# Performance work log

Hardware: AMD Instinct MI355X
Metric: run time of the kernel (lower is better)

## Reference

```python
import jax, jax.numpy as jnp
import numpy as np

D_MODEL = 1024
NHEAD = 16
HEAD_DIM = D_MODEL // NHEAD
SCALE = HEAD_DIM ** (-0.5)


def setup_inputs() -> dict:
    key = jax.random.key(0)
    k1, k2, k3 = jax.random.split(key, 3)
    B, T, C = 2, 2048, D_MODEL
    x = jax.random.normal(k1, (B, T, C), dtype=jnp.float32)
    W_qkv = jax.random.normal(k2, (3 * C, C), dtype=jnp.float32) * (C ** -0.5)
    b_qkv = jnp.zeros((3 * C,), dtype=jnp.float32)
    W_out = jax.random.normal(k3, (C, C), dtype=jnp.float32) * (C ** -0.5)
    b_out = jnp.zeros((C,), dtype=jnp.float32)
    return {"x": x, "W_qkv": W_qkv, "b_qkv": b_qkv, "W_out": W_out, "b_out": b_out}


def reference(x, W_qkv, b_qkv, W_out, b_out):
    B, T, C = x.shape
    H, hd = NHEAD, HEAD_DIM
    qkv = x @ W_qkv.T + b_qkv
    qkv = qkv.reshape(B, T, 3, H, hd).transpose(2, 0, 3, 1, 4)
    q, k, v = qkv[0], qkv[1], qkv[2]
    # scaled dot-product scores: (B,H,T,T)
    attn = jnp.einsum('bhqd,bhkd->bhqk', q, k) * SCALE
    # causal mask (is_causal=True): lower-triangular allowed
    causal = jnp.tril(jnp.ones((T, T), dtype=bool))
    attn = jnp.where(causal[None, None, :, :], attn, -jnp.inf)
    attn = jax.nn.softmax(attn, axis=-1)
    # (B,H,T,hd) -> (B,T,C)
    out = jnp.einsum('bhqk,bhkd->bhqd', attn, v)
    out = out.transpose(0, 2, 1, 3).reshape(B, T, C)
    out = out @ W_out.T + b_out
    return out
```

## Files before the change

kernel.cpp:

```cpp
#include <hip/hip_runtime.h>
#include <hip/hip_bf16.h>
#include <stdint.h>

#define D_MODEL 1024
#define NHEAD   16
#define HEAD_DIM 64
#define BATCH   2
#define SEQ     2048
#define M_TOK   (BATCH*SEQ)
#define N_QKV   (3*D_MODEL)
#define KDIM    1024
#define Q_SCALE (0.125f * 1.44269504088896f)

typedef __bf16 bf16_t;
typedef bf16_t bf16x8 __attribute__((ext_vector_type(8)));
typedef bf16_t bf16x4 __attribute__((ext_vector_type(4)));
typedef float  f32x4  __attribute__((ext_vector_type(4)));
typedef float  f32x16 __attribute__((ext_vector_type(16)));
typedef unsigned u32x4 __attribute__((ext_vector_type(4)));

__device__ __forceinline__ void gl_lds16(const void* g, void* l) {
    __builtin_amdgcn_global_load_lds(
        (__attribute__((address_space(1))) void*)(void*)(const_cast<void*>(g)),
        (__attribute__((address_space(3))) void*)l, 16, 0, 0);
}

__device__ __forceinline__ unsigned cvtpk_bf16(float a, float b) {
    unsigned r;
    asm("v_cvt_pk_bf16_f32 %0, %1, %2" : "=v"(r) : "v"(a), "v"(b));
    return r;
}

#define N4_X  (M_TOK * KDIM / 4)
#define N4_W1 (N_QKV * KDIM / 4)
#define N4_W2 (D_MODEL * KDIM / 4)
__global__ void convert_all(const float* __restrict__ x,
                            const float* __restrict__ w1,
                            const float* __restrict__ w2,
                            bf16_t* __restrict__ ox,
                            bf16_t* __restrict__ o1,
                            bf16_t* __restrict__ o2) {
    int t = blockIdx.x * blockDim.x + threadIdx.x;
    const float* src;
    bf16_t* dst;
    int off;
    if (t < N4_X)                { src = x;  dst = ox; off = t; }
    else if (t < N4_X + N4_W1)   { src = w1; dst = o1; off = t - N4_X; }
    else                         { src = w2; dst = o2; off = t - N4_X - N4_W1; }
    float4 v = reinterpret_cast<const float4*>(src)[off];
    bf16x4 o = { (bf16_t)v.x, (bf16_t)v.y, (bf16_t)v.z, (bf16_t)v.w };
    reinterpret_cast<bf16x4*>(dst)[off] = o;
}

template <int MODE, int TN>
__global__ __launch_bounds__(256) void gemm_bt(
    const bf16_t* __restrict__ A,
    const bf16_t* __restrict__ Bw,
    const float*  __restrict__ bias,
    int N,
    bf16_t* __restrict__ qkv_out,
    bf16_t* __restrict__ vt_out,
    float*  __restrict__ f32_out)
{
    constexpr int NJ = TN / 32;
    __shared__ bf16_t As[128 * 64];
    __shared__ bf16_t Bs[TN * 64];

    const int cpx = gridDim.x >> 3;
    const int bid = (blockIdx.x & 7) * cpx + (blockIdx.x >> 3);

    const int nbn = N / TN;
    const int bm = bid / nbn;
    const int bn = bid % nbn;
    const int m0 = bm * 128, n0 = bn * TN;
    const int tid = threadIdx.x, wave = tid >> 6, lane = tid & 63;
    const int wr = wave >> 1, wc = wave & 1;

    f32x4 acc[4][NJ] = {};

    const int srow = lane >> 3;
    const int scol = ((lane & 7) ^ srow) * 8;
    const bf16_t* gA0 = A  + (size_t)(m0 + wave * 32 + srow) * KDIM + scol;
    const bf16_t* gB0 = Bw + (size_t)(n0 + wave * (TN / 4) + srow) * KDIM + scol;
    bf16_t* lA0 = &As[(wave * 32) * 64];
    bf16_t* lB0 = &Bs[(wave * (TN / 4)) * 64];

    const int fr = lane & 15;
    const int kq = lane >> 4;

    for (int k0 = 0; k0 < KDIM; k0 += 64) {
#pragma unroll
        for (int c = 0; c < 4; c++)
            gl_lds16(gA0 + (size_t)(c * 8) * KDIM + k0, lA0 + (c * 8) * 64);
#pragma unroll
        for (int c = 0; c < TN / 32; c++)
            gl_lds16(gB0 + (size_t)(c * 8) * KDIM + k0, lB0 + (c * 8) * 64);
        __syncthreads();

        bf16x8 af[2][4], bfr[2][NJ];
#pragma unroll
        for (int kk = 0; kk < 2; kk++) {
            const int ch = (((kk << 2) | kq) ^ (fr & 7)) * 8;
#pragma unroll
            for (int i = 0; i < 4; i++)
                af[kk][i] = *reinterpret_cast<const bf16x8*>(
                    &As[(wr * 64 + i * 16 + fr) * 64 + ch]);
#pragma unroll
            for (int j = 0; j < NJ; j++)
                bfr[kk][j] = *reinterpret_cast<const bf16x8*>(
                    &Bs[(wc * (TN / 2) + j * 16 + fr) * 64 + ch]);
        }
        __builtin_amdgcn_s_setprio(1);
#pragma unroll
        for (int i = 0; i < 4; i++)
#pragma unroll
            for (int j = 0; j < NJ; j++) {
                acc[i][j] = __builtin_amdgcn_mfma_f32_16x16x32_bf16(
                    af[0][i], bfr[0][j], acc[i][j], 0, 0, 0);
                acc[i][j] = __builtin_amdgcn_mfma_f32_16x16x32_bf16(
                    af[1][i], bfr[1][j], acc[i][j], 0, 0, 0);
            }
        __builtin_amdgcn_s_setprio(0);
        __syncthreads();
    }

#pragma unroll
    for (int i = 0; i < 4; i++) {
#pragma unroll
        for (int j = 0; j < NJ; j++) {
            const int col = n0 + wc * (TN / 2) + j * 16 + fr;
            const float bv = bias[col];
            const int row0 = m0 + wr * 64 + i * 16 + kq * 4;
            if (MODE == 1) {
#pragma unroll
                for (int r = 0; r < 4; r++)
                    f32_out[(size_t)(row0 + r) * N + col] = acc[i][j][r] + bv;
            } else if (col < 1024) {
#pragma unroll
                for (int r = 0; r < 4; r++)
                    qkv_out[(size_t)(row0 + r) * N_QKV + col] =
                        (bf16_t)((acc[i][j][r] + bv) * Q_SCALE);
            } else if (col < 2048) {
#pragma unroll
                for (int r = 0; r < 4; r++)
                    qkv_out[(size_t)(row0 + r) * N_QKV + col] =
                        (bf16_t)(acc[i][j][r] + bv);
            } else {
                const int d = col & 63, hh = (col >> 6) & 15;
                const int bb = row0 >> 11, t0 = row0 & 2047;
                const int t0p = t0 ^ ((((t0 >> 2) ^ (t0 >> 3)) & 1) ? 12 : 0);
                bf16x4 pv = { (bf16_t)(acc[i][j][0] + bv),
                              (bf16_t)(acc[i][j][1] + bv),
                              (bf16_t)(acc[i][j][2] + bv),
                              (bf16_t)(acc[i][j][3] + bv) };
                *reinterpret_cast<bf16x4*>(
                    &vt_out[((size_t)((bb * NHEAD + hh) * HEAD_DIM + d)) * SEQ + t0p]) = pv;
            }
        }
    }
}

__global__ __launch_bounds__(256, 4) void attn_fwd(
    const bf16_t* __restrict__ qkv,
    const bf16_t* __restrict__ Vt,
    bf16_t* __restrict__ O)
{
    __shared__ bf16_t Ks[2][64 * 64];
    __shared__ bf16_t Vs[2][64 * 64];

    const int nqt = SEQ / 64;
    const int nbh = BATCH * NHEAD;
    const int qt = (nqt - 1) - (blockIdx.x / nbh);
    const int bh = blockIdx.x % nbh;
    const int b = bh >> 4, h = bh & 15;
    const int q0 = qt * 64;
    const int tid = threadIdx.x, wave = tid >> 6, lane = tid & 63;
    const int group = wave >> 1;
    const int w4 = wave & 1;
    const int ln31 = lane & 31;
    const int ag = lane >> 5;
    const int akey = ln31 & 7;

    bf16x8 qf[4];
    {
        const size_t qrow = (size_t)(b * SEQ + q0 + w4 * 32 + ln31);
        const bf16_t* qp = qkv + qrow * N_QKV + h * 64 + ag * 8;
        qf[0] = *reinterpret_cast<const bf16x8*>(qp);
        qf[1] = *reinterpret_cast<const bf16x8*>(qp + 16);
        qf[2] = *reinterpret_cast<const bf16x8*>(qp + 32);
        qf[3] = *reinterpret_cast<const bf16x8*>(qp + 48);
    }

    f32x16 acc[2] = {};
    float l_part = 0.f;

    const int srow = lane >> 3;
    const int scol = ((lane & 7) ^ srow) * 8;
    const bf16_t* gK = qkv + (size_t)(b * SEQ) * N_QKV + (D_MODEL + h * 64);
    const bf16_t* gV = Vt + (size_t)(bh * 64) * SEQ;

    const int nh0 = (qt + 2) >> 1;
    const int my_n = (group == 0) ? nh0 : (qt + 1 - nh0);
    const int base_t = (group == 0) ? 0 : nh0;

    for (int it = 0; it < nh0; ++it) {
        const bool act = (it < my_n);
        const int g_it = base_t + it;
        const int kv0 = g_it * 64;
        if (act) {
#pragma unroll
            for (int c = 0; c < 4; c++) {
                const int row = w4 * 32 + c * 8 + srow;
                gl_lds16(gK + (size_t)(kv0 + row) * N_QKV + scol,
                         &Ks[group][(w4 * 32 + c * 8) * 64]);
                gl_lds16(gV + (size_t)row * SEQ + kv0 + scol,
                         &Vs[group][(w4 * 32 + c * 8) * 64]);
            }
        }
        __syncthreads();

        if (act) {
#pragma unroll
            for (int m = 0; m < 2; m++) {
                f32x16 s = {};
                __builtin_amdgcn_s_setprio(1);
#pragma unroll
                for (int c = 0; c < 4; c++) {
                    bf16x8 kf = *reinterpret_cast<const bf16x8*>(
                        &Ks[group][(m * 32 + ln31) * 64 + (((c * 2 + ag) ^ akey) * 8)]);
                    s = __builtin_amdgcn_mfma_f32_32x32x16_bf16(kf, qf[c], s, 0, 0, 0);
                }
                __builtin_amdgcn_s_setprio(0);

                if (g_it == qt) {
                    const int qg = w4 * 32 + ln31;
#pragma unroll
                    for (int r = 0; r < 16; r++) {
                        const int kvl = m * 32 + (r & 3) + 8 * (r >> 2) + 4 * ag;
                        if (kvl > qg) s[r] = -1e30f;
                    }
                }

                float rs = 0.f;
#pragma unroll
                for (int r = 0; r < 16; r++) {
                    const float p = exp2f(s[r]);
                    s[r] = p;
                    rs += p;
                }
                l_part += rs;

                __builtin_amdgcn_s_setprio(1);
#pragma unroll
                for (int c2 = 0; c2 < 2; c2++) {
                    const int bs = c2 * 8;
                    u32x4 bw = { cvtpk_bf16(s[bs + 0], s[bs + 1]),
                                 cvtpk_bf16(s[bs + 2], s[bs + 3]),
                                 cvtpk_bf16(s[bs + 4], s[bs + 5]),
                                 cvtpk_bf16(s[bs + 6], s[bs + 7]) };
                    bf16x8 pb = __builtin_bit_cast(bf16x8, bw);
                    const int C = 4 * m + 2 * c2 + ag;
#pragma unroll
                    for (int dm = 0; dm < 2; dm++) {
                        bf16x8 vf = *reinterpret_cast<const bf16x8*>(
                            &Vs[group][(dm * 32 + ln31) * 64 + ((C ^ akey) * 8)]);
                        acc[dm] = __builtin_amdgcn_mfma_f32_32x32x16_bf16(
                            vf, pb, acc[dm], 0, 0, 0);
                    }
                }
                __builtin_amdgcn_s_setprio(0);
            }
        }
        __syncthreads();
    }

    float* Cf = reinterpret_cast<float*>(&Ks[0][0]);
    const int cb = w4 * 2112;
    if (group == 1) {
#pragma unroll
        for (int dm = 0; dm < 2; dm++)
#pragma unroll
            for (int r = 0; r < 16; r++)
                Cf[cb + (dm * 16 + r) * 64 + lane] = acc[dm][r];
        Cf[cb + 2048 + lane] = l_part;
    }
    __syncthreads();
    if (group == 0) {
#pragma unroll
        for (int dm = 0; dm < 2; dm++)
#pragma unroll
            for (int r = 0; r < 16; r++)
                acc[dm][r] += Cf[cb + (dm * 16 + r) * 64 + lane];
        l_part += Cf[cb + 2048 + lane];

        l_part += __shfl_xor(l_part, 32);
        const float inv = 1.0f / l_part;
        const size_t rowq = (size_t)(b * SEQ + q0 + w4 * 32 + ln31);
#pragma unroll
        for (int dm = 0; dm < 2; dm++)
#pragma unroll
            for (int k = 0; k < 4; k++) {
                const int d0 = dm * 32 + 8 * k + 4 * ag;
                bf16x4 ov = { (bf16_t)(acc[dm][4 * k + 0] * inv),
                              (bf16_t)(acc[dm][4 * k + 1] * inv),
                              (bf16_t)(acc[dm][4 * k + 2] * inv),
                              (bf16_t)(acc[dm][4 * k + 3] * inv) };
                *reinterpret_cast<bf16x4*>(&O[rowq * D_MODEL + h * 64 + d0]) = ov;
            }
    }
}

extern "C" void kernel_launch(void* const* d_in, const int* in_sizes, int n_in,
                              void* d_out, int out_size, void* d_ws, size_t ws_size,
                              hipStream_t stream) {
    (void)in_sizes; (void)n_in; (void)out_size; (void)ws_size;
    const float* x    = (const float*)d_in[0];
    const float* Wqkv = (const float*)d_in[1];
    const float* bqkv = (const float*)d_in[2];
    const float* Wout = (const float*)d_in[3];
    const float* bout = (const float*)d_in[4];
    float* out = (float*)d_out;

    char* ws = (char*)d_ws;
    size_t off = 0;
    bf16_t* x_bf    = (bf16_t*)(ws + off); off += (size_t)M_TOK * KDIM * 2;
    bf16_t* wqkv_bf = (bf16_t*)(ws + off); off += (size_t)N_QKV * KDIM * 2;
    bf16_t* wout_bf = (bf16_t*)(ws + off); off += (size_t)D_MODEL * KDIM * 2;
    bf16_t* qkv     = (bf16_t*)(ws + off); off += (size_t)M_TOK * N_QKV * 2;
    bf16_t* vt      = (bf16_t*)(ws + off); off += (size_t)BATCH * NHEAD * HEAD_DIM * SEQ * 2;
    bf16_t* o_bf    = (bf16_t*)(ws + off); off += (size_t)M_TOK * D_MODEL * 2;

    convert_all<<<(N4_X + N4_W1 + N4_W2) / 256, 256, 0, stream>>>(
        x, Wqkv, Wout, x_bf, wqkv_bf, wout_bf);

    gemm_bt<0, 128><<<(M_TOK / 128) * (N_QKV / 128), 256, 0, stream>>>(
        x_bf, wqkv_bf, bqkv, N_QKV, qkv, vt, nullptr);

    attn_fwd<<<BATCH * NHEAD * (SEQ / 64), 256, 0, stream>>>(qkv, vt, o_bf);

    gemm_bt<1, 64><<<(M_TOK / 128) * (D_MODEL / 64), 256, 0, stream>>>(
        o_bf, wout_bf, bout, D_MODEL, nullptr, nullptr, out);
}
```

Before: 96.59 us.

## Process 128-query tiles per block with two 4-wave KV-split groups

The attention kernel now uses 512-thread blocks that each cover 128 query rows instead of 64. The 8 waves form two groups that split the causal KV range evenly (qt2+1 tiles each), so the idle iterations from the old uneven split go away. Each wave loads half as many K/V rows per tile into a per-group LDS buffer. The trade-off is half as many blocks, larger blocks that may limit occupancy, and a per-tile global-position mask check on the diagonal tiles.

After: 102.0 us. 5.7% more time.

```diff
diff --git a/kernel.cpp b/kernel.cpp
--- a/kernel.cpp
+++ b/kernel.cpp
@@ -160,26 +160,31 @@
     }
 }
 
-__global__ __launch_bounds__(256, 4) void attn_fwd(
+__global__ __launch_bounds__(512, 4) void attn_fwd(
     const bf16_t* __restrict__ qkv,
     const bf16_t* __restrict__ Vt,
     bf16_t* __restrict__ O)
 {
-    __shared__ bf16_t Ks[2][64 * 64];
-    __shared__ bf16_t Vs[2][64 * 64];
-
-    const int nqt = SEQ / 64;
+    __shared__ __align__(16) char smem_raw[33792];
+    bf16_t* KsB = (bf16_t*)smem_raw;
+    bf16_t* VsB = (bf16_t*)(smem_raw + 16384);
+    float*  Cf  = (float*)smem_raw;
+
+    const int nq2 = SEQ / 128;
     const int nbh = BATCH * NHEAD;
-    const int qt = (nqt - 1) - (blockIdx.x / nbh);
+    const int qt2 = (nq2 - 1) - (blockIdx.x / nbh);
     const int bh = blockIdx.x % nbh;
     const int b = bh >> 4, h = bh & 15;
-    const int q0 = qt * 64;
+    const int q0 = qt2 * 128;
     const int tid = threadIdx.x, wave = tid >> 6, lane = tid & 63;
-    const int group = wave >> 1;
-    const int w4 = wave & 1;
+    const int group = wave >> 2;
+    const int w4 = wave & 3;
     const int ln31 = lane & 31;
     const int ag = lane >> 5;
     const int akey = ln31 & 7;
+
+    bf16_t* Ks = KsB + group * 4096;
+    bf16_t* Vs = VsB + group * 4096;
 
     bf16x8 qf[4];
     {
@@ -199,82 +204,75 @@
     const bf16_t* gK = qkv + (size_t)(b * SEQ) * N_QKV + (D_MODEL + h * 64);
     const bf16_t* gV = Vt + (size_t)(bh * 64) * SEQ;
 
-    const int nh0 = (qt + 2) >> 1;
-    const int my_n = (group == 0) ? nh0 : (qt + 1 - nh0);
-    const int base_t = (group == 0) ? 0 : nh0;
-
-    for (int it = 0; it < nh0; ++it) {
-        const bool act = (it < my_n);
+    const int ntpg = qt2 + 1;
+    const int base_t = group * ntpg;
+
+    for (int it = 0; it < ntpg; ++it) {
         const int g_it = base_t + it;
         const int kv0 = g_it * 64;
-        if (act) {
-#pragma unroll
-            for (int c = 0; c < 4; c++) {
-                const int row = w4 * 32 + c * 8 + srow;
-                gl_lds16(gK + (size_t)(kv0 + row) * N_QKV + scol,
-                         &Ks[group][(w4 * 32 + c * 8) * 64]);
-                gl_lds16(gV + (size_t)row * SEQ + kv0 + scol,
-                         &Vs[group][(w4 * 32 + c * 8) * 64]);
-            }
+#pragma unroll
+        for (int c = 0; c < 2; c++) {
+            const int row = w4 * 16 + c * 8 + srow;
+            gl_lds16(gK + (size_t)(kv0 + row) * N_QKV + scol,
+                     Ks + (w4 * 16 + c * 8) * 64);
+            gl_lds16(gV + (size_t)row * SEQ + kv0 + scol,
+                     Vs + (w4 * 16 + c * 8) * 64);
         }
         __syncthreads();
 
-        if (act) {
-#pragma unroll
-            for (int m = 0; m < 2; m++) {
-                f32x16 s = {};
-                __builtin_amdgcn_s_setprio(1);
-#pragma unroll
-                for (int c = 0; c < 4; c++) {
-                    bf16x8 kf = *reinterpret_cast<const bf16x8*>(
-                        &Ks[group][(m * 32 + ln31) * 64 + (((c * 2 + ag) ^ akey) * 8)]);
-                    s = __builtin_amdgcn_mfma_f32_32x32x16_bf16(kf, qf[c], s, 0, 0, 0);
+#pragma unroll
+        for (int m = 0; m < 2; m++) {
+            f32x16 s = {};
+            __builtin_amdgcn_s_setprio(1);
+#pragma unroll
+            for (int c = 0; c < 4; c++) {
+                bf16x8 kf = *reinterpret_cast<const bf16x8*>(
+                    &Ks[(m * 32 + ln31) * 64 + (((c * 2 + ag) ^ akey) * 8)]);
+                s = __builtin_amdgcn_mfma_f32_32x32x16_bf16(kf, qf[c], s, 0, 0, 0);
+            }
+            __builtin_amdgcn_s_setprio(0);
+
+            if (g_it >= 2 * qt2) {
+                const int qg = q0 + w4 * 32 + ln31;
+#pragma unroll
+                for (int r = 0; r < 16; r++) {
+                    const int kvg = kv0 + m * 32 + (r & 3) + 8 * (r >> 2) + 4 * ag;
+                    if (kvg > qg) s[r] = -1e30f;
                 }
-                __builtin_amdgcn_s_setprio(0);
-
-                if (g_it == qt) {
-                    const int qg = w4 * 32 + ln31;
-#pragma unroll
-                    for (int r = 0; r < 16; r++) {
-                        const int kvl = m * 32 + (r & 3) + 8 * (r >> 2) + 4 * ag;
-                        if (kvl > qg) s[r] = -1e30f;
-                    }
+            }
+
+            float rs = 0.f;
+#pragma unroll
+            for (int r = 0; r < 16; r++) {
+                const float p = exp2f(s[r]);
+                s[r] = p;
+                rs += p;
+            }
+            l_part += rs;
+
+            __builtin_amdgcn_s_setprio(1);
+#pragma unroll
+            for (int c2 = 0; c2 < 2; c2++) {
+                const int bs = c2 * 8;
+                u32x4 bw = { cvtpk_bf16(s[bs + 0], s[bs + 1]),
+                             cvtpk_bf16(s[bs + 2], s[bs + 3]),
+                             cvtpk_bf16(s[bs + 4], s[bs + 5]),
+                             cvtpk_bf16(s[bs + 6], s[bs + 7]) };
+                bf16x8 pb = __builtin_bit_cast(bf16x8, bw);
+                const int C = 4 * m + 2 * c2 + ag;
+#pragma unroll
+                for (int dm = 0; dm < 2; dm++) {
+                    bf16x8 vf = *reinterpret_cast<const bf16x8*>(
+                        &Vs[(dm * 32 + ln31) * 64 + ((C ^ akey) * 8)]);
+                    acc[dm] = __builtin_amdgcn_mfma_f32_32x32x16_bf16(
+                        vf, pb, acc[dm], 0, 0, 0);
                 }
-
-                float rs = 0.f;
-#pragma unroll
-                for (int r = 0; r < 16; r++) {
-                    const float p = exp2f(s[r]);
-                    s[r] = p;
-                    rs += p;
-                }
-                l_part += rs;
-
-                __builtin_amdgcn_s_setprio(1);
-#pragma unroll
-                for (int c2 = 0; c2 < 2; c2++) {
-                    const int bs = c2 * 8;
-                    u32x4 bw = { cvtpk_bf16(s[bs + 0], s[bs + 1]),
-                                 cvtpk_bf16(s[bs + 2], s[bs + 3]),
-                                 cvtpk_bf16(s[bs + 4], s[bs + 5]),
-                                 cvtpk_bf16(s[bs + 6], s[bs + 7]) };
-                    bf16x8 pb = __builtin_bit_cast(bf16x8, bw);
-                    const int C = 4 * m + 2 * c2 + ag;
-#pragma unroll
-                    for (int dm = 0; dm < 2; dm++) {
-                        bf16x8 vf = *reinterpret_cast<const bf16x8*>(
-                            &Vs[group][(dm * 32 + ln31) * 64 + ((C ^ akey) * 8)]);
-                        acc[dm] = __builtin_amdgcn_mfma_f32_32x32x16_bf16(
-                            vf, pb, acc[dm], 0, 0, 0);
-                    }
-                }
-                __builtin_amdgcn_s_setprio(0);
-            }
+            }
+            __builtin_amdgcn_s_setprio(0);
         }
         __syncthreads();
     }
 
-    float* Cf = reinterpret_cast<float*>(&Ks[0][0]);
     const int cb = w4 * 2112;
     if (group == 1) {
 #pragma unroll
@@ -336,7 +334,7 @@
     gemm_bt<0, 128><<<(M_TOK / 128) * (N_QKV / 128), 256, 0, stream>>>(
         x_bf, wqkv_bf, bqkv, N_QKV, qkv, vt, nullptr);
 
-    attn_fwd<<<BATCH * NHEAD * (SEQ / 64), 256, 0, stream>>>(qkv, vt, o_bf);
+    attn_fwd<<<(SEQ / 128) * BATCH * NHEAD, 512, 0, stream>>>(qkv, vt, o_bf);
 
     gemm_bt<1, 64><<<(M_TOK / 128) * (D_MODEL / 64), 256, 0, stream>>>(
         o_bf, wout_bf, bout, D_MODEL, nullptr, nullptr, out);
```
